# Kernel optimization log

Measured on AMD Instinct MI355X. Metric: run time of the kernel, lower is better.

## Reference

```python
import jax, jax.numpy as jnp
import numpy as np

D = 768      # feature_dim
HD = 768     # hidden_dim
NH = 4       # num_heads
B, T1, T2 = 4, 128, 128
LN_EPS = 1e-5

def setup_inputs() -> dict:
    key = jax.random.key(0)
    ks = jax.random.split(key, 12)
    s = 0.02
    return {
        'speech_features': jax.random.normal(ks[0], (B, T1, D), jnp.float32),
        'phoneme_features': jax.random.normal(ks[1], (B, T2, D), jnp.float32),
        # per-head attention MLP: Linear(2D->HD), ReLU, Linear(HD->1); stacked over heads
        'W1': jax.random.normal(ks[2], (NH, 2 * D, HD), jnp.float32) * s,
        'b1': jnp.zeros((NH, HD), jnp.float32),
        'w2': jax.random.normal(ks[3], (NH, HD), jnp.float32) * s,
        'b2': jnp.zeros((NH,), jnp.float32),
        # fusion: Linear(2D->2HD), ReLU, Linear(2HD->D), LayerNorm(D)
        'Wf1': jax.random.normal(ks[4], (2 * D, 2 * HD), jnp.float32) * s,
        'bf1': jnp.zeros((2 * HD,), jnp.float32),
        'Wf2': jax.random.normal(ks[5], (2 * HD, D), jnp.float32) * s,
        'bf2': jnp.zeros((D,), jnp.float32),
        'ln_g': jnp.ones((D,), jnp.float32),
        'ln_b': jnp.zeros((D,), jnp.float32),
    }

def reference(speech_features, phoneme_features, W1, b1, w2, b2, Wf1, bf1, Wf2, bf2, ln_g, ln_b):
    d = speech_features.shape[-1]
    # Decompose Linear(cat([speech_t, phoneme])) = speech@W1[:d] + phoneme@W1[d:] + b1
    Wx, Wy = W1[:, :d, :], W1[:, d:, :]
    sx = jnp.einsum('btd,ndh->nbth', speech_features, Wx)   # [NH,B,T1,HD]
    py = jnp.einsum('bsd,ndh->nbsh', phoneme_features, Wy)  # [NH,B,T2,HD]
    hidden = jax.nn.relu(sx[:, :, :, None, :] + py[:, :, None, :, :]
                         + b1[:, None, None, None, :])      # [NH,B,T1,T2,HD]
    scores = jnp.einsum('nbtsh,nh->nbts', hidden, w2) + b2[:, None, None, None]
    attn = jax.nn.softmax(scores, axis=-1).mean(axis=0)     # [B,T1,T2]
    context = jnp.einsum('bts,bsd->btd', attn, phoneme_features)  # [B,T1,D]
    fused = jnp.concatenate([speech_features, context], axis=-1)  # [B,T1,2D]
    # dropout is identity in eval mode
    h = jax.nn.relu(fused @ Wf1 + bf1)
    out = h @ Wf2 + bf2
    mu = out.mean(axis=-1, keepdims=True)
    var = ((out - mu) ** 2).mean(axis=-1, keepdims=True)
    out = (out - mu) * jax.lax.rsqrt(var + LN_EPS) * ln_g + ln_b
    return out.mean(axis=1)  # [B,D]
```

## Files before the change

kernel.cpp:

```cpp
#include <hip/hip_runtime.h>
#include <cstddef>


#define D_  768
#define HD_ 768
#define NH_ 4
#define B_  4
#define T1_ 128
#define T2_ 128
#define M_  (B_*T1_)
#define LN_EPS_ 1e-5f

typedef unsigned short u16;
typedef unsigned int u32;
typedef _Float16 f16;
typedef _Float16 f16x2 __attribute__((ext_vector_type(2)));
typedef __bf16 bf16x8 __attribute__((ext_vector_type(8)));
typedef float f32x4 __attribute__((ext_vector_type(4)));

__device__ __forceinline__ u16 f2bf(float f) {
    union { float f; unsigned int u; } v; v.f = f;
    unsigned int u = v.u + (0x7FFFu + ((v.u >> 16) & 1u));
    return (u16)(u >> 16);
}
__device__ __forceinline__ u32 pack_bf2(float lo, float hi) {
    return (u32)f2bf(lo) | ((u32)f2bf(hi) << 16);
}
__device__ __forceinline__ u16 f16bits(f16 h) {
    return __builtin_bit_cast(unsigned short, h);
}
__device__ __forceinline__ f16x2 bcast2(u32 u) {
    return __builtin_bit_cast(f16x2, u);
}
__device__ __forceinline__ u32 splat2(u16 h) { return (u32)h * 0x10001u; }

template<bool RELU, int MODE, bool AF32>
__device__ __forceinline__ void gemm_mfma_body(
    const void* __restrict__ Av, int lda,
    const u16* __restrict__ Bt, int ldb,
    const float* __restrict__ bias,
    void* __restrict__ C, int ldc, int K, int m0, int n0)
{
    __shared__ __align__(16) u16 As[64][40];
    __shared__ __align__(16) u16 Bs[64][40];
    __shared__ u16 Ts[MODE == 3 ? 64 : 1][MODE == 3 ? 68 : 1];

    const int tid = threadIdx.x;
    const int row = tid >> 2;
    const int kq  = (tid & 3) << 3;
    const int lane = tid & 63;
    const int w  = tid >> 6;
    const int wr = (w >> 1) << 5;
    const int wc = (w & 1) << 5;
    const int l16 = lane & 15;
    const int lk8 = (lane >> 4) << 3;
    const int r4  = (lane >> 4) << 2;

    const u16*   aptr16 = (const u16*)Av + (size_t)(m0 + row) * lda + kq;
    const float* aptrf  = (const float*)Av + (size_t)(m0 + row) * lda + kq;
    const u16*   bptr   = Bt + (size_t)(n0 + row) * ldb + kq;

    f32x4 acc00 = {0.f,0.f,0.f,0.f}, acc01 = {0.f,0.f,0.f,0.f};
    f32x4 acc10 = {0.f,0.f,0.f,0.f}, acc11 = {0.f,0.f,0.f,0.f};

    auto loadA = [&](int k0) -> uint4 {
        if (AF32) {
            float4 ax = *(const float4*)(aptrf + k0);
            float4 ay = *(const float4*)(aptrf + k0 + 4);
            uint4 r;
            r.x = pack_bf2(ax.x, ax.y); r.y = pack_bf2(ax.z, ax.w);
            r.z = pack_bf2(ay.x, ay.y); r.w = pack_bf2(ay.z, ay.w);
            return r;
        }
        return *(const uint4*)(aptr16 + k0);
    };

    uint4 a_nxt = loadA(0);
    uint4 b_nxt = *(const uint4*)bptr;

    for (int k0 = 0; k0 < K; k0 += 32) {
        __syncthreads();
        *(uint4*)&As[row][kq] = a_nxt;
        *(uint4*)&Bs[row][kq] = b_nxt;
        if (k0 + 32 < K) {
            a_nxt = loadA(k0 + 32);
            b_nxt = *(const uint4*)(bptr + k0 + 32);
        }
        __syncthreads();
        bf16x8 af0 = *(const bf16x8*)&As[wr + l16][lk8];
        bf16x8 af1 = *(const bf16x8*)&As[wr + 16 + l16][lk8];
        bf16x8 bf0 = *(const bf16x8*)&Bs[wc + l16][lk8];
        bf16x8 bf1 = *(const bf16x8*)&Bs[wc + 16 + l16][lk8];
        acc00 = __builtin_amdgcn_mfma_f32_16x16x32_bf16(af0, bf0, acc00, 0, 0, 0);
        acc01 = __builtin_amdgcn_mfma_f32_16x16x32_bf16(af0, bf1, acc01, 0, 0, 0);
        acc10 = __builtin_amdgcn_mfma_f32_16x16x32_bf16(af1, bf0, acc10, 0, 0, 0);
        acc11 = __builtin_amdgcn_mfma_f32_16x16x32_bf16(af1, bf1, acc11, 0, 0, 0);
    }

#define EPI_FRAG(ACC, MF, NF)                                                  \
    {                                                                          \
        const int gcol = n0 + wc + (NF)*16 + l16;                              \
        const float bv = bias ? bias[gcol] : 0.f;                              \
        float v_[4];                                                           \
        _Pragma("unroll")                                                      \
        for (int r = 0; r < 4; r++) {                                          \
            float v = ACC[r] + bv;                                             \
            if (RELU) v = fmaxf(v, 0.f);                                       \
            v_[r] = v;                                                         \
        }                                                                      \
        const int lr0 = wr + (MF)*16 + r4;                                     \
        if (MODE == 3) {                                                       \
            const int lc = wc + (NF)*16 + l16;                                 \
            _Pragma("unroll")                                                  \
            for (int r = 0; r < 4; r++) Ts[lc][lr0 + r] = f16bits((f16)v_[r]); \
        } else {                                                               \
            _Pragma("unroll")                                                  \
            for (int r = 0; r < 4; r++) {                                      \
                const size_t off = (size_t)(m0 + lr0 + r) * ldc + gcol;        \
                if (MODE == 0) ((float*)C)[off] = v_[r];                       \
                else if (MODE == 1) ((u16*)C)[off] = f2bf(v_[r]);              \
                else ((u16*)C)[off] = f16bits((f16)v_[r]);                     \
            }                                                                  \
        }                                                                      \
    }
    EPI_FRAG(acc00, 0, 0) EPI_FRAG(acc01, 0, 1)
    EPI_FRAG(acc10, 1, 0) EPI_FRAG(acc11, 1, 1)
#undef EPI_FRAG

    if (MODE == 3) {
        __syncthreads();
        u16* cb = (u16*)C + (size_t)(m0 >> 7) * (768 * 128) + (m0 & 127);
#pragma unroll
        for (int u = 0; u < 4; u++) {
            const int i = tid + u * 256;
            const int hl = i >> 4;
            const int s4 = (i & 15) << 2;
            ushort4 o;
            o.x = Ts[hl][s4 + 0]; o.y = Ts[hl][s4 + 1];
            o.z = Ts[hl][s4 + 2]; o.w = Ts[hl][s4 + 3];
            *(ushort4*)(cb + (size_t)(n0 + hl) * 128 + s4) = o;
        }
    }
}

__global__ __launch_bounds__(256) void prep_kernel(
    const float* __restrict__ W1, const float* __restrict__ Wf1,
    const float* __restrict__ Wf2,
    u16* __restrict__ w1t, u16* __restrict__ wf1t, u16* __restrict__ wf2t)
{
    const int tid = threadIdx.x;
    int bid = blockIdx.x;
    const float* in; u16* outp; int tx, ty;
    if (bid < 4608) {
        const int z = bid / 1152, r = bid % 1152;
        tx = r % 24; ty = r / 24;
        in = W1 + (size_t)z * 1536 * 768; outp = w1t + (size_t)z * 768 * 1536;
    } else if (bid < 6912) {
        const int r = bid - 4608;
        tx = r % 48; ty = r / 48;
        in = Wf1; outp = wf1t;
    } else {
        const int r = bid - 6912;
        tx = r % 24; ty = r / 24;
        in = Wf2; outp = wf2t;
    }
    const int C = (bid >= 4608 && bid < 6912) ? 1536 : 768;
    const int c0 = tx * 32, r0 = ty * 32;
    __shared__ float tile[32][33];
    const int tr = tid >> 3, tc = (tid & 7) << 2;
    float4 v = *(const float4*)(in + (size_t)(r0 + tr) * C + c0 + tc);
    tile[tr][tc] = v.x; tile[tr][tc + 1] = v.y;
    tile[tr][tc + 2] = v.z; tile[tr][tc + 3] = v.w;
    __syncthreads();
    ushort4 o;
    o.x = f2bf(tile[tc + 0][tr]); o.y = f2bf(tile[tc + 1][tr]);
    o.z = f2bf(tile[tc + 2][tr]); o.w = f2bf(tile[tc + 3][tr]);
    *(ushort4*)(outp + (size_t)(c0 + tr) * 1536 + r0 + tc) = o;
}

__global__ __launch_bounds__(256) void gemm_sxpy_kernel(
    const float* __restrict__ sp, const float* __restrict__ ph,
    const u16* __restrict__ w1t, const float* __restrict__ b1,
    u16* __restrict__ sxf, u16* __restrict__ pyt)
{
    const int z = blockIdx.z;
    const int n = z & 3;
    const bool ispy = z >= 4;
    const u16* Bt = w1t + (size_t)n * 768 * 1536 + (ispy ? 768 : 0);
    if (!ispy) {
        gemm_mfma_body<false, 2, true>(sp, 768, Bt, 1536, b1 + n * HD_,
                                       sxf + (size_t)n * M_ * HD_, HD_, 768,
                                       blockIdx.y * 64, blockIdx.x * 64);
    } else {
        gemm_mfma_body<false, 3, true>(ph, 768, Bt, 1536, nullptr,
                                       pyt + (size_t)n * 4 * 768 * 128, 0, 768,
                                       blockIdx.y * 64, blockIdx.x * 64);
    }
}

template<bool RELU, int MODE>
__global__ __launch_bounds__(256) void gemm_mfma_kernel(
    const u16* __restrict__ A, int lda,
    const u16* __restrict__ Bt, int ldb,
    const float* __restrict__ bias,
    void* __restrict__ C, int ldc, int K)
{
    gemm_mfma_body<RELU, MODE, false>(A, lda, Bt, ldb, bias, C, ldc, K,
                                      blockIdx.y * 64, blockIdx.x * 64);
}

__global__ __launch_bounds__(256) void scores_ctx_kernel(
    const u16* __restrict__ sxf,
    const u16* __restrict__ pyt,
    const float* __restrict__ w2,
    const float* __restrict__ phon,
    const float* __restrict__ speech,
    u16* __restrict__ fused)
{
    const int bid = blockIdx.x;
    const int b = bid >> 7, t = bid & 127;
    const int m = b * 128 + t;
    const int tid = threadIdx.x, lane = tid & 63, w = tid >> 6;

    __shared__ __align__(16) f16x2 sxs[4][768];
    __shared__ __align__(16) f16x2 w2s[4][768];
    __shared__ float attn4[4][128];
    __shared__ float attn[128];

#pragma unroll
    for (int q = 0; q < 3; q++) {
        const int u = lane + 64 * q;
        const int h4 = u * 4;
        ushort4 v = *(const ushort4*)(sxf + ((size_t)(w * 512 + m)) * 768 + h4);
        sxs[w][h4 + 0] = bcast2(splat2(v.x));
        sxs[w][h4 + 1] = bcast2(splat2(v.y));
        sxs[w][h4 + 2] = bcast2(splat2(v.z));
        sxs[w][h4 + 3] = bcast2(splat2(v.w));
        float4 wv = *(const float4*)(w2 + w * 768 + h4);
        w2s[w][h4 + 0] = bcast2(splat2(f16bits((f16)wv.x)));
        w2s[w][h4 + 1] = bcast2(splat2(f16bits((f16)wv.y)));
        w2s[w][h4 + 2] = bcast2(splat2(f16bits((f16)wv.z)));
        w2s[w][h4 + 3] = bcast2(splat2(f16bits((f16)wv.w)));
    }

    const f16x2* pypanel = (const f16x2*)(pyt + ((size_t)((w << 2) | b)) * 768 * 128) + lane;
    const f16x2 z2 = {(f16)0, (f16)0};

    float acc0 = 0.f, acc1 = 0.f;

    f16x2 b0[16], b1[16];
#pragma unroll
    for (int j = 0; j < 16; j++) b0[j] = pypanel[(size_t)j * 64];
#pragma unroll
    for (int j = 0; j < 16; j++) b1[j] = pypanel[(size_t)(16 + j) * 64];

    for (int hc = 0; hc < 768; hc += 32) {
        f16x2 a4[4] = {z2, z2, z2, z2};
#pragma unroll
        for (int j = 0; j < 16; j++) {
            f16x2 r_ = __builtin_elementwise_max(sxs[w][hc + j] + b0[j], z2);
            a4[j & 3] = __builtin_elementwise_fma(r_, w2s[w][hc + j], a4[j & 3]);
        }
        if (hc + 32 < 768) {
#pragma unroll
            for (int j = 0; j < 16; j++) b0[j] = pypanel[(size_t)(hc + 32 + j) * 64];
        }
#pragma unroll
        for (int j = 0; j < 16; j++) {
            f16x2 r_ = __builtin_elementwise_max(sxs[w][hc + 16 + j] + b1[j], z2);
            a4[j & 3] = __builtin_elementwise_fma(r_, w2s[w][hc + 16 + j], a4[j & 3]);
        }
        if (hc + 48 < 768) {
#pragma unroll
            for (int j = 0; j < 16; j++) b1[j] = pypanel[(size_t)(hc + 48 + j) * 64];
        }
#pragma unroll
        for (int k = 0; k < 4; k++) {
            acc0 += (float)a4[k].x;
            acc1 += (float)a4[k].y;
        }
    }

    float mx = fmaxf(acc0, acc1);
#pragma unroll
    for (int off = 32; off; off >>= 1) mx = fmaxf(mx, __shfl_xor(mx, off, 64));
    const float e0 = expf(acc0 - mx), e1 = expf(acc1 - mx);
    float sm = e0 + e1;
#pragma unroll
    for (int off = 32; off; off >>= 1) sm += __shfl_xor(sm, off, 64);
    const float inv = 0.25f / sm;
    float2 pr; pr.x = e0 * inv; pr.y = e1 * inv;
    *(float2*)&attn4[w][2 * lane] = pr;
    __syncthreads();

    if (tid < 128)
        attn[tid] = attn4[0][tid] + attn4[1][tid] + attn4[2][tid] + attn4[3][tid];
    __syncthreads();

    const float* ph = phon + (size_t)b * 128 * 768;
#pragma unroll
    for (int j = 0; j < 3; j++) {
        const int d = tid + 256 * j;
        float acc = 0.f;
#pragma unroll 8
        for (int s = 0; s < 128; s++)
            acc = fmaf(attn[s], ph[(size_t)s * 768 + d], acc);
        fused[(size_t)m * 1536 + d] = f2bf(speech[(size_t)m * 768 + d]);
        fused[(size_t)m * 1536 + 768 + d] = f2bf(acc);
    }
}

__global__ __launch_bounds__(256) void ln_fused_kernel(
    const float* __restrict__ x, const float* __restrict__ g,
    const float* __restrict__ lb, float* __restrict__ out)
{
    const int b = blockIdx.x / 3, c = blockIdx.x % 3;
    const int tid = threadIdx.x, lane = tid & 63, w = tid >> 6;
    __shared__ float rs[T1_];
    __shared__ float Sred[4];

    float prsum = 0.f;
    for (int i = 0; i < 32; i++) {
        const int row = w * 32 + i;
        const float4* x4 = (const float4*)(x + ((size_t)(b * T1_ + row)) * D_);
        float s = 0.f, ss = 0.f;
#pragma unroll
        for (int j = 0; j < 3; j++) {
            float4 v = x4[j * 64 + lane];
            s += v.x + v.y + v.z + v.w;
            ss += v.x * v.x + v.y * v.y + v.z * v.z + v.w * v.w;
        }
#pragma unroll
        for (int off = 32; off; off >>= 1) {
            s += __shfl_xor(s, off, 64);
            ss += __shfl_xor(ss, off, 64);
        }
        if (lane == 0) {
            const float mu = s * (1.f / D_);
            const float var = ss * (1.f / D_) - mu * mu;
            const float r = rsqrtf(var + LN_EPS_);
            rs[row] = r;
            prsum += mu * r;
        }
    }
    if (lane == 0) Sred[w] = prsum;
    __syncthreads();
    const float S = Sred[0] + Sred[1] + Sred[2] + Sred[3];
    const float* xb = x + (size_t)b * T1_ * D_;
    const int d = c * 256 + tid;
    float acc = 0.f;
#pragma unroll 8
    for (int t = 0; t < T1_; t++)
        acc = fmaf(xb[(size_t)t * D_ + d], rs[t], acc);
    out[b * D_ + d] = g[d] * (acc - S) * (1.f / T1_) + lb[d];
}

extern "C" void kernel_launch(void* const* d_in, const int* in_sizes, int n_in,
                              void* d_out, int out_size, void* d_ws, size_t ws_size,
                              hipStream_t stream)
{
    const float* speech = (const float*)d_in[0];
    const float* phon   = (const float*)d_in[1];
    const float* W1     = (const float*)d_in[2];
    const float* b1     = (const float*)d_in[3];
    const float* w2     = (const float*)d_in[4];
    const float* Wf1    = (const float*)d_in[6];
    const float* bf1    = (const float*)d_in[7];
    const float* Wf2    = (const float*)d_in[8];
    const float* bf2    = (const float*)d_in[9];
    const float* ln_g   = (const float*)d_in[10];
    const float* ln_b   = (const float*)d_in[11];
    float* out = (float*)d_out;

    char* w = (char*)d_ws;
    auto alloc = [&](size_t bytes) { char* p = w; w += (bytes + 1023) & ~(size_t)1023; return p; };
    u16* w1t    = (u16*)alloc((size_t)NH_ * 768 * 1536 * 2);
    u16* wf1t   = (u16*)alloc((size_t)1536 * 1536 * 2);
    u16* wf2t   = (u16*)alloc((size_t)768 * 1536 * 2);
    u16* sxf    = (u16*)alloc((size_t)NH_ * M_ * HD_ * 2);
    u16* pyt    = (u16*)alloc((size_t)NH_ * B_ * 768 * 128 * 2);
    u16* fusedb = (u16*)alloc((size_t)M_ * 2 * D_ * 2);
    u16* hbuf   = (u16*)alloc((size_t)M_ * 2 * HD_ * 2);
    float* outpre = (float*)alloc((size_t)M_ * D_ * 4);

    hipLaunchKernelGGL(prep_kernel, dim3(8064), dim3(256), 0, stream,
                       W1, Wf1, Wf2, w1t, wf1t, wf2t);
    hipLaunchKernelGGL(gemm_sxpy_kernel, dim3(HD_ / 64, M_ / 64, 8), dim3(256), 0, stream,
                       speech, phon, w1t, b1, sxf, pyt);
    hipLaunchKernelGGL(scores_ctx_kernel, dim3(512), dim3(256), 0, stream,
                       sxf, pyt, w2, phon, speech, fusedb);
    hipLaunchKernelGGL((gemm_mfma_kernel<true, 1>), dim3(2 * HD_ / 64, M_ / 64), dim3(256), 0, stream,
                       fusedb, 2 * D_, wf1t, 1536, bf1, hbuf, 2 * HD_, 2 * D_);
    hipLaunchKernelGGL((gemm_mfma_kernel<false, 0>), dim3(D_ / 64, M_ / 64), dim3(256), 0, stream,
                       hbuf, 2 * HD_, wf2t, 1536, bf2, outpre, D_, 2 * HD_);
    hipLaunchKernelGGL(ln_fused_kernel, dim3(12), dim3(256), 0, stream,
                       outpre, ln_g, ln_b, out);
}
```

Measured before the change: 127.8 us.

## Process two query rows per block in scores kernel with vectorized LDS reads

The scores/context kernel now handles two speech timesteps per block using 512 threads (8 waves: 4 heads x 2 rows), halving the grid to 256 blocks. w2 is loaded once per head and shared by both rows. The inner loop reads sx and w2 from shared memory as 16-byte vectors instead of scalar f16x2 loads. This cuts LDS instruction count and redundant setup, at the cost of half as many blocks on a 256-CU device and more LDS per block. The py panel loads are not shared between the two rows.

```diff
diff --git a/kernel.cpp b/kernel.cpp
--- a/kernel.cpp
+++ b/kernel.cpp
@@ -209,7 +209,7 @@
                                       blockIdx.y * 64, blockIdx.x * 64);
 }
 
-__global__ __launch_bounds__(256) void scores_ctx_kernel(
+__global__ __launch_bounds__(512) void scores_ctx_kernel(
     const u16* __restrict__ sxf,
     const u16* __restrict__ pyt,
     const float* __restrict__ w2,
@@ -218,32 +218,37 @@
     u16* __restrict__ fused)
 {
     const int bid = blockIdx.x;
-    const int b = bid >> 7, t = bid & 127;
-    const int m = b * 128 + t;
-    const int tid = threadIdx.x, lane = tid & 63, w = tid >> 6;
-
-    __shared__ __align__(16) f16x2 sxs[4][768];
+    const int b = bid >> 6, t0 = (bid & 63) * 2;
+    const int m0 = b * 128 + t0;
+    const int tid = threadIdx.x, lane = tid & 63;
+    const int W = tid >> 6;
+    const int n = W >> 1, r = W & 1;
+
+    __shared__ __align__(16) f16x2 sxs[4][2][768];
     __shared__ __align__(16) f16x2 w2s[4][768];
-    __shared__ float attn4[4][128];
-    __shared__ float attn[128];
+    __shared__ float attn4[4][2][128];
+    __shared__ float attn[2][128];
 
 #pragma unroll
     for (int q = 0; q < 3; q++) {
         const int u = lane + 64 * q;
         const int h4 = u * 4;
-        ushort4 v = *(const ushort4*)(sxf + ((size_t)(w * 512 + m)) * 768 + h4);
-        sxs[w][h4 + 0] = bcast2(splat2(v.x));
-        sxs[w][h4 + 1] = bcast2(splat2(v.y));
-        sxs[w][h4 + 2] = bcast2(splat2(v.z));
-        sxs[w][h4 + 3] = bcast2(splat2(v.w));
-        float4 wv = *(const float4*)(w2 + w * 768 + h4);
-        w2s[w][h4 + 0] = bcast2(splat2(f16bits((f16)wv.x)));
-        w2s[w][h4 + 1] = bcast2(splat2(f16bits((f16)wv.y)));
-        w2s[w][h4 + 2] = bcast2(splat2(f16bits((f16)wv.z)));
-        w2s[w][h4 + 3] = bcast2(splat2(f16bits((f16)wv.w)));
-    }
-
-    const f16x2* pypanel = (const f16x2*)(pyt + ((size_t)((w << 2) | b)) * 768 * 128) + lane;
+        ushort4 v = *(const ushort4*)(sxf + ((size_t)(n * 512 + m0 + r)) * 768 + h4);
+        sxs[n][r][h4 + 0] = bcast2(splat2(v.x));
+        sxs[n][r][h4 + 1] = bcast2(splat2(v.y));
+        sxs[n][r][h4 + 2] = bcast2(splat2(v.z));
+        sxs[n][r][h4 + 3] = bcast2(splat2(v.w));
+        if (r == 0) {
+            float4 wv = *(const float4*)(w2 + n * 768 + h4);
+            w2s[n][h4 + 0] = bcast2(splat2(f16bits((f16)wv.x)));
+            w2s[n][h4 + 1] = bcast2(splat2(f16bits((f16)wv.y)));
+            w2s[n][h4 + 2] = bcast2(splat2(f16bits((f16)wv.z)));
+            w2s[n][h4 + 3] = bcast2(splat2(f16bits((f16)wv.w)));
+        }
+    }
+    __syncthreads();
+
+    const f16x2* pypanel = (const f16x2*)(pyt + ((size_t)((n << 2) | b)) * 768 * 128) + lane;
     const f16x2 z2 = {(f16)0, (f16)0};
 
     float acc0 = 0.f, acc1 = 0.f;
@@ -253,23 +258,30 @@
     for (int j = 0; j < 16; j++) b0[j] = pypanel[(size_t)j * 64];
 #pragma unroll
     for (int j = 0; j < 16; j++) b1[j] = pypanel[(size_t)(16 + j) * 64];
+
+    auto compute = [&](const f16x2 (&buf)[16], int hbase, f16x2 (&a4)[4]) {
+#pragma unroll
+        for (int j4 = 0; j4 < 16; j4 += 4) {
+            uint4 sau = *(const uint4*)&sxs[n][r][hbase + j4];
+            uint4 wvu = *(const uint4*)&w2s[n][hbase + j4];
+            const u32 sa_[4] = {sau.x, sau.y, sau.z, sau.w};
+            const u32 wv_[4] = {wvu.x, wvu.y, wvu.z, wvu.w};
+#pragma unroll
+            for (int j = 0; j < 4; j++) {
+                f16x2 r_ = __builtin_elementwise_max(bcast2(sa_[j]) + buf[j4 + j], z2);
+                a4[j] = __builtin_elementwise_fma(r_, bcast2(wv_[j]), a4[j]);
+            }
+        }
+    };
 
     for (int hc = 0; hc < 768; hc += 32) {
         f16x2 a4[4] = {z2, z2, z2, z2};
-#pragma unroll
-        for (int j = 0; j < 16; j++) {
-            f16x2 r_ = __builtin_elementwise_max(sxs[w][hc + j] + b0[j], z2);
-            a4[j & 3] = __builtin_elementwise_fma(r_, w2s[w][hc + j], a4[j & 3]);
-        }
+        compute(b0, hc, a4);
         if (hc + 32 < 768) {
 #pragma unroll
             for (int j = 0; j < 16; j++) b0[j] = pypanel[(size_t)(hc + 32 + j) * 64];
         }
-#pragma unroll
-        for (int j = 0; j < 16; j++) {
-            f16x2 r_ = __builtin_elementwise_max(sxs[w][hc + 16 + j] + b1[j], z2);
-            a4[j & 3] = __builtin_elementwise_fma(r_, w2s[w][hc + 16 + j], a4[j & 3]);
-        }
+        compute(b1, hc + 16, a4);
         if (hc + 48 < 768) {
 #pragma unroll
             for (int j = 0; j < 16; j++) b1[j] = pypanel[(size_t)(hc + 48 + j) * 64];
@@ -290,23 +302,30 @@
     for (int off = 32; off; off >>= 1) sm += __shfl_xor(sm, off, 64);
     const float inv = 0.25f / sm;
     float2 pr; pr.x = e0 * inv; pr.y = e1 * inv;
-    *(float2*)&attn4[w][2 * lane] = pr;
+    *(float2*)&attn4[n][r][2 * lane] = pr;
     __syncthreads();
 
-    if (tid < 128)
-        attn[tid] = attn4[0][tid] + attn4[1][tid] + attn4[2][tid] + attn4[3][tid];
+    if (tid < 256) {
+        const int rr = tid >> 7, s = tid & 127;
+        attn[rr][s] = attn4[0][rr][s] + attn4[1][rr][s] + attn4[2][rr][s] + attn4[3][rr][s];
+    }
     __syncthreads();
 
-    const float* ph = phon + (size_t)b * 128 * 768;
-#pragma unroll
-    for (int j = 0; j < 3; j++) {
-        const int d = tid + 256 * j;
-        float acc = 0.f;
+    {
+        const int rr = tid >> 8;
+        const int dbase = tid & 255;
+        const int m = m0 + rr;
+        const float* ph = phon + (size_t)b * 128 * 768;
+#pragma unroll
+        for (int j = 0; j < 3; j++) {
+            const int d = dbase + 256 * j;
+            float acc = 0.f;
 #pragma unroll 8
-        for (int s = 0; s < 128; s++)
-            acc = fmaf(attn[s], ph[(size_t)s * 768 + d], acc);
-        fused[(size_t)m * 1536 + d] = f2bf(speech[(size_t)m * 768 + d]);
-        fused[(size_t)m * 1536 + 768 + d] = f2bf(acc);
+            for (int s = 0; s < 128; s++)
+                acc = fmaf(attn[rr][s], ph[(size_t)s * 768 + d], acc);
+            fused[(size_t)m * 1536 + d] = f2bf(speech[(size_t)m * 768 + d]);
+            fused[(size_t)m * 1536 + 768 + d] = f2bf(acc);
+        }
     }
 }
 
@@ -387,7 +406,7 @@
                        W1, Wf1, Wf2, w1t, wf1t, wf2t);
     hipLaunchKernelGGL(gemm_sxpy_kernel, dim3(HD_ / 64, M_ / 64, 8), dim3(256), 0, stream,
                        speech, phon, w1t, b1, sxf, pyt);
-    hipLaunchKernelGGL(scores_ctx_kernel, dim3(512), dim3(256), 0, stream,
+    hipLaunchKernelGGL(scores_ctx_kernel, dim3(256), dim3(512), 0, stream,
                        sxf, pyt, w2, phon, speech, fusedb);
     hipLaunchKernelGGL((gemm_mfma_kernel<true, 1>), dim3(2 * HD_ / 64, M_ / 64), dim3(256), 0, stream,
                        fusedb, 2 * D_, wf1t, 1536, bf1, hbuf, 2 * HD_, 2 * D_);
```

New measurement: 128.5 us. Within noise of the previous version (+0.6%).
